# Kernel optimization log

Hardware: AMD Instinct MI355X
Metric: run time of the kernel (lower is better)

Reference implementation:

```python
import jax, jax.numpy as jnp
import numpy as np

N = 100000   # nodes
E = 640000   # directed edges
D = 128      # feature dim
C = 2        # classes


def setup_inputs() -> dict:
    key = jax.random.key(0)
    ks = jax.random.split(key, 7)
    s = 1.0 / np.sqrt(D)
    return {
        "x": jax.random.normal(ks[0], (N, D), jnp.float32),
        "edge_index": jax.random.randint(ks[1], (2, E), 0, N, jnp.int32),
        "W1": jax.random.normal(ks[2], (D, D), jnp.float32) * s,
        "b1": jnp.zeros((D,), jnp.float32),
        "W2": jax.random.normal(ks[3], (D, D), jnp.float32) * s,
        "b2": jnp.zeros((D,), jnp.float32),
        "Wfc": jax.random.normal(ks[4], (D, C), jnp.float32) * s,
        "bfc": jnp.zeros((C,), jnp.float32),
    }


def _gcn_conv(h, src, dst, W, b, n):
    """PyG GCNConv: y = D^{-1/2}(A+I)D^{-1/2} (h @ W) + b."""
    h = h @ W  # [N, D_out]
    loop = jnp.arange(n, dtype=src.dtype)
    s = jnp.concatenate([src, loop])
    d = jnp.concatenate([dst, loop])
    # degree of (A + I) counted at destination
    deg = jax.ops.segment_sum(jnp.ones_like(d, jnp.float32), d, num_segments=n)
    dinv = jax.lax.rsqrt(jnp.maximum(deg, 1.0))  # deg >= 1 via self loops
    norm = dinv[s] * dinv[d]                      # [E+N]
    msg = h[s] * norm[:, None]                    # gather + scale
    out = jax.ops.segment_sum(msg, d, num_segments=n)  # scatter-add
    return out + b


def reference(x, edge_index, W1, b1, W2, b2, Wfc, bfc):
    src, dst = edge_index[0], edge_index[1]
    n = x.shape[0]
    h = jax.nn.relu(_gcn_conv(x, src, dst, W1, b1, n))  # dropout = identity (eval)
    h = jax.nn.relu(_gcn_conv(h, src, dst, W2, b2, n))
    return h @ Wfc + bfc  # [N, 2] logits
```

## Files before the change

### kernel.cpp

```cpp
#include <hip/hip_runtime.h>
#include <hip/hip_bf16.h>

#define D 128

typedef __bf16 bf16x8 __attribute__((ext_vector_type(8)));
typedef float f32x4 __attribute__((ext_vector_type(4)));



__global__ void prep_kernel(const float* __restrict__ W1, const float* __restrict__ W2,
                            __bf16* __restrict__ pw, int* __restrict__ counts, int n) {
    int b = blockIdx.x;
    if (b < 128) {
        int t = b * 256 + threadIdx.x;
        int which = t >> 14, idx = t & 16383;
        const float* W = which ? W2 : W1;
        float w = W[idx];
        int k = idx >> 7, nn = idx & 127;
        int ks = which ? (((k & 15) << 3) | (k >> 4)) : k;
        int ntile = nn >> 4, nl = nn & 15;
        int kchunk = ks >> 5, quad = (ks >> 3) & 3, j = ks & 7;
        int o = (((ntile * 4 + kchunk) * 64 + quad * 16 + nl) << 3) + j;
        pw[(size_t)which * 16384 + o] = (__bf16)w;
    } else {
        int i0 = (b - 128) * 1024 + threadIdx.x * 4;
        if (i0 + 4 <= n) {
            *(int4*)(counts + i0) = make_int4(0, 0, 0, 0);
        } else {
            for (int i = i0; i < n; i++) counts[i] = 0;
        }
    }
}


__global__ void mega1_kernel(const float* __restrict__ X, const __bf16* __restrict__ PW,
                             __bf16* __restrict__ Zs, int nrows, int gb,
                             const int* __restrict__ dst, int* __restrict__ counts,
                             int* __restrict__ eoff, int e) {
    __shared__ bf16x8 sB[2048];
    int b = blockIdx.x;
    if (b >= gb) {
        int i0 = ((b - gb) * 256 + threadIdx.x) * 4;
        if (i0 + 4 <= e) {
            int4 d4 = *(const int4*)(dst + i0);
            int4 o;
            o.x = atomicAdd(&counts[d4.x], 1);
            o.y = atomicAdd(&counts[d4.y], 1);
            o.z = atomicAdd(&counts[d4.z], 1);
            o.w = atomicAdd(&counts[d4.w], 1);
            *(int4*)(eoff + i0) = o;
        } else {
            for (int i = i0; i < e; i++) eoff[i] = atomicAdd(&counts[dst[i]], 1);
        }
        return;
    }
    int t = threadIdx.x;
    const bf16x8* PW8 = (const bf16x8*)PW;
#pragma unroll
    for (int i = 0; i < 8; i++) sB[t + 256 * i] = PW8[t + 256 * i];

    int wave = t >> 6, lane = t & 63;
    int qm = lane & 15, quad = lane >> 4;
    int r0 = b * 64 + wave * 16;
    int row = r0 + qm;
    bool valid = row < nrows;
    const float* xr = X + (size_t)row * D + quad * 8;

    bf16x8 ahi[4], alo[4];
#pragma unroll
    for (int c = 0; c < 4; c++) {
        float4 zf = {0.f, 0.f, 0.f, 0.f};
        float4 xa = valid ? ((const float4*)(xr + c * 32))[0] : zf;
        float4 xb = valid ? ((const float4*)(xr + c * 32))[1] : zf;
        float xs[8] = {xa.x, xa.y, xa.z, xa.w, xb.x, xb.y, xb.z, xb.w};
        bf16x8 h, l;
#pragma unroll
        for (int j = 0; j < 8; j++) {
            float v = xs[j];
            __bf16 hh = (__bf16)v;
            h[j] = hh;
            l[j] = (__bf16)(v - (float)hh);
        }
        ahi[c] = h; alo[c] = l;
    }

    f32x4 acc[8];
#pragma unroll
    for (int nt = 0; nt < 8; nt++) acc[nt] = (f32x4){0.f, 0.f, 0.f, 0.f};

    __syncthreads();

#pragma unroll
    for (int c = 0; c < 4; c++) {
#pragma unroll
        for (int nt = 0; nt < 8; nt++) {
            bf16x8 bb = sB[(nt * 4 + c) * 64 + lane];
            acc[nt] = __builtin_amdgcn_mfma_f32_16x16x32_bf16(ahi[c], bb, acc[nt], 0, 0, 0);
            acc[nt] = __builtin_amdgcn_mfma_f32_16x16x32_bf16(alo[c], bb, acc[nt], 0, 0, 0);
        }
    }

#pragma unroll
    for (int reg = 0; reg < 4; reg++) {
        int orow = r0 + quad * 4 + reg;
        if (orow < nrows) {
            bf16x8 o;
#pragma unroll
            for (int nt = 0; nt < 8; nt++) o[nt] = (__bf16)acc[nt][reg];
            *(bf16x8*)(Zs + (size_t)orow * D + qm * 8) = o;
        }
    }
}


__global__ void scan_part(const int* __restrict__ counts, int* __restrict__ partial, int n) {
    __shared__ int sm[256];
    int b = blockIdx.x, t = threadIdx.x;
    int base = b * 2048 + t * 8;
    int s = 0;
#pragma unroll
    for (int j = 0; j < 8; j++) { int idx = base + j; if (idx < n) s += counts[idx]; }
    sm[t] = s; __syncthreads();
    for (int off = 128; off > 0; off >>= 1) { if (t < off) sm[t] += sm[t + off]; __syncthreads(); }
    if (t == 0) partial[b] = sm[0];
}

__global__ void scan_top(int* partial, int nb) {
    __shared__ int sm[256];
    int t = threadIdx.x;
    int v = (t < nb) ? partial[t] : 0;
    sm[t] = v; __syncthreads();
    for (int off = 1; off < 256; off <<= 1) {
        int u = (t >= off) ? sm[t - off] : 0;
        __syncthreads();
        sm[t] += u;
        __syncthreads();
    }
    if (t < nb) partial[t] = sm[t] - v;
}

__global__ void scan_down(const int* __restrict__ counts, const int* __restrict__ blockoff,
                          int* __restrict__ row_ptr, float* __restrict__ dinv, int n) {
    __shared__ int sm[256];
    int b = blockIdx.x, t = threadIdx.x;
    int base = b * 2048 + t * 8;
    int c[8], local[8];
    int s = 0;
#pragma unroll
    for (int j = 0; j < 8; j++) {
        int idx = base + j;
        c[j] = (idx < n) ? counts[idx] : 0;
        local[j] = s; s += c[j];
        if (idx < n) dinv[idx] = rsqrtf((float)(c[j] + 1));
    }
    sm[t] = s; __syncthreads();
    int own = s;
    for (int off = 1; off < 256; off <<= 1) {
        int u = (t >= off) ? sm[t - off] : 0;
        __syncthreads();
        sm[t] += u;
        __syncthreads();
    }
    int basev = blockoff[b] + sm[t] - own;
#pragma unroll
    for (int j = 0; j < 8; j++) { int idx = base + j; if (idx < n) row_ptr[idx] = basev + local[j]; }
}


__global__ void fill_kernel(const int* __restrict__ src, const int* __restrict__ dst,
                            const int* __restrict__ row_ptr, const int* __restrict__ eoff,
                            const float* __restrict__ dinv, int2* __restrict__ csr, int e) {
    int i0 = (blockIdx.x * 256 + threadIdx.x) * 4;
    if (i0 + 4 <= e) {
        int4 s4 = *(const int4*)(src + i0);
        int4 d4 = *(const int4*)(dst + i0);
        int4 o4 = *(const int4*)(eoff + i0);
        int p0 = row_ptr[d4.x] + o4.x;
        int p1 = row_ptr[d4.y] + o4.y;
        int p2 = row_ptr[d4.z] + o4.z;
        int p3 = row_ptr[d4.w] + o4.w;
        float w0 = dinv[s4.x] * dinv[d4.x];
        float w1 = dinv[s4.y] * dinv[d4.y];
        float w2 = dinv[s4.z] * dinv[d4.z];
        float w3 = dinv[s4.w] * dinv[d4.w];
        csr[p0] = make_int2(s4.x, __float_as_int(w0));
        csr[p1] = make_int2(s4.y, __float_as_int(w1));
        csr[p2] = make_int2(s4.z, __float_as_int(w2));
        csr[p3] = make_int2(s4.w, __float_as_int(w3));
    } else {
        for (int i = i0; i < e; i++) {
            int s = src[i], d = dst[i];
            int pos = row_ptr[d] + eoff[i];
            csr[pos] = make_int2(s, __float_as_int(dinv[s] * dinv[d]));
        }
    }
}


__global__ void gemm2_mfma(const __bf16* __restrict__ Hs, const __bf16* __restrict__ PW,
                           __bf16* __restrict__ Zs, int nrows) {
    __shared__ bf16x8 sB[2048];
    int t = threadIdx.x;
    const bf16x8* PW8 = (const bf16x8*)PW;
#pragma unroll
    for (int i = 0; i < 8; i++) sB[t + 256 * i] = PW8[t + 256 * i];

    int wave = t >> 6, lane = t & 63;
    int qm = lane & 15, quad = lane >> 4;
    int r0 = blockIdx.x * 64 + wave * 16;
    int row = r0 + qm;
    bool valid = row < nrows;
    const __bf16* hr = Hs + (size_t)row * D + quad * 8;

    bf16x8 a[4];
#pragma unroll
    for (int c = 0; c < 4; c++) {
        bf16x8 z8 = {};
        a[c] = valid ? *(const bf16x8*)(hr + c * 32) : z8;
    }

    f32x4 acc[8];
#pragma unroll
    for (int nt = 0; nt < 8; nt++) acc[nt] = (f32x4){0.f, 0.f, 0.f, 0.f};

    __syncthreads();

#pragma unroll
    for (int c = 0; c < 4; c++) {
#pragma unroll
        for (int nt = 0; nt < 8; nt++) {
            bf16x8 b = sB[(nt * 4 + c) * 64 + lane];
            acc[nt] = __builtin_amdgcn_mfma_f32_16x16x32_bf16(a[c], b, acc[nt], 0, 0, 0);
        }
    }

#pragma unroll
    for (int reg = 0; reg < 4; reg++) {
        int orow = r0 + quad * 4 + reg;
        if (orow < nrows) {
            bf16x8 o;
#pragma unroll
            for (int nt = 0; nt < 8; nt++) o[nt] = (__bf16)acc[nt][reg];
            *(bf16x8*)(Zs + (size_t)orow * D + qm * 8) = o;
        }
    }
}


__global__ void agg1_kernel(const __bf16* __restrict__ Zs, const int* __restrict__ row_ptr,
                            const int* __restrict__ counts, const int2* __restrict__ csr,
                            const float* __restrict__ dinv, const float* __restrict__ bias,
                            __bf16* __restrict__ Hs, int n) {
    int t = blockIdx.x * 256 + threadIdx.x;
    int v = t >> 4, c = t & 15;
    if (v >= n) return;
    float dv = dinv[v];
    const bf16x8* Z8 = (const bf16x8*)Zs;
    bf16x8 zc = Z8[(size_t)v * 16 + c];
    float sw = dv * dv;
    float acc[8];
#pragma unroll
    for (int j = 0; j < 8; j++) acc[j] = (float)zc[j] * sw;
    int start = row_ptr[v], cnt = counts[v];
    int i = 0;
    for (; i + 4 <= cnt; i += 4) {
        int2 e0 = csr[start + i], e1 = csr[start + i + 1];
        int2 e2 = csr[start + i + 2], e3 = csr[start + i + 3];
        bf16x8 m0 = Z8[(size_t)e0.x * 16 + c];
        bf16x8 m1 = Z8[(size_t)e1.x * 16 + c];
        bf16x8 m2 = Z8[(size_t)e2.x * 16 + c];
        bf16x8 m3 = Z8[(size_t)e3.x * 16 + c];
        float w0 = __int_as_float(e0.y), w1 = __int_as_float(e1.y);
        float w2 = __int_as_float(e2.y), w3 = __int_as_float(e3.y);
#pragma unroll
        for (int j = 0; j < 8; j++) acc[j] = fmaf(w0, (float)m0[j], acc[j]);
#pragma unroll
        for (int j = 0; j < 8; j++) acc[j] = fmaf(w1, (float)m1[j], acc[j]);
#pragma unroll
        for (int j = 0; j < 8; j++) acc[j] = fmaf(w2, (float)m2[j], acc[j]);
#pragma unroll
        for (int j = 0; j < 8; j++) acc[j] = fmaf(w3, (float)m3[j], acc[j]);
    }
    for (; i < cnt; i++) {
        int2 e0 = csr[start + i];
        float w0 = __int_as_float(e0.y);
        bf16x8 m0 = Z8[(size_t)e0.x * 16 + c];
#pragma unroll
        for (int j = 0; j < 8; j++) acc[j] = fmaf(w0, (float)m0[j], acc[j]);
    }
    bf16x8 o;
#pragma unroll
    for (int j = 0; j < 8; j++) o[j] = (__bf16)fmaxf(acc[j] + bias[j * 16 + c], 0.f);
    ((bf16x8*)Hs)[(size_t)v * 16 + c] = o;
}


__global__ void agg2_fc_kernel(const __bf16* __restrict__ Zs, const int* __restrict__ row_ptr,
                               const int* __restrict__ counts, const int2* __restrict__ csr,
                               const float* __restrict__ dinv, const float* __restrict__ bias,
                               const float* __restrict__ Wfc, const float* __restrict__ bfc,
                               float* __restrict__ out, int n) {
    int t = blockIdx.x * 256 + threadIdx.x;
    int v = t >> 4, c = t & 15;
    if (v >= n) return;
    float dv = dinv[v];
    const bf16x8* Z8 = (const bf16x8*)Zs;
    bf16x8 zc = Z8[(size_t)v * 16 + c];
    float sw = dv * dv;
    float acc[8];
#pragma unroll
    for (int j = 0; j < 8; j++) acc[j] = (float)zc[j] * sw;
    int start = row_ptr[v], cnt = counts[v];
    int i = 0;
    for (; i + 4 <= cnt; i += 4) {
        int2 e0 = csr[start + i], e1 = csr[start + i + 1];
        int2 e2 = csr[start + i + 2], e3 = csr[start + i + 3];
        bf16x8 m0 = Z8[(size_t)e0.x * 16 + c];
        bf16x8 m1 = Z8[(size_t)e1.x * 16 + c];
        bf16x8 m2 = Z8[(size_t)e2.x * 16 + c];
        bf16x8 m3 = Z8[(size_t)e3.x * 16 + c];
        float w0 = __int_as_float(e0.y), w1 = __int_as_float(e1.y);
        float w2 = __int_as_float(e2.y), w3 = __int_as_float(e3.y);
#pragma unroll
        for (int j = 0; j < 8; j++) acc[j] = fmaf(w0, (float)m0[j], acc[j]);
#pragma unroll
        for (int j = 0; j < 8; j++) acc[j] = fmaf(w1, (float)m1[j], acc[j]);
#pragma unroll
        for (int j = 0; j < 8; j++) acc[j] = fmaf(w2, (float)m2[j], acc[j]);
#pragma unroll
        for (int j = 0; j < 8; j++) acc[j] = fmaf(w3, (float)m3[j], acc[j]);
    }
    for (; i < cnt; i++) {
        int2 e0 = csr[start + i];
        float w0 = __int_as_float(e0.y);
        bf16x8 m0 = Z8[(size_t)e0.x * 16 + c];
#pragma unroll
        for (int j = 0; j < 8; j++) acc[j] = fmaf(w0, (float)m0[j], acc[j]);
    }
    float a0 = 0.f, a1 = 0.f;
#pragma unroll
    for (int j = 0; j < 8; j++) {
        int p = j * 16 + c;
        float hj = fmaxf(acc[j] + bias[p], 0.f);
        a0 = fmaf(hj, Wfc[p * 2], a0);
        a1 = fmaf(hj, Wfc[p * 2 + 1], a1);
    }
#pragma unroll
    for (int off = 8; off > 0; off >>= 1) {
        a0 += __shfl_down(a0, off, 16);
        a1 += __shfl_down(a1, off, 16);
    }
    if (c == 0) {
        out[(size_t)v * 2 + 0] = a0 + bfc[0];
        out[(size_t)v * 2 + 1] = a1 + bfc[1];
    }
}


extern "C" void kernel_launch(void* const* d_in, const int* in_sizes, int n_in,
                              void* d_out, int out_size, void* d_ws, size_t ws_size,
                              hipStream_t stream) {
    const float* x   = (const float*)d_in[0];
    const int*   ei  = (const int*)d_in[1];
    const float* W1  = (const float*)d_in[2];
    const float* b1  = (const float*)d_in[3];
    const float* W2  = (const float*)d_in[4];
    const float* b2  = (const float*)d_in[5];
    const float* Wfc = (const float*)d_in[6];
    const float* bfc = (const float*)d_in[7];
    float* out = (float*)d_out;

    int n = in_sizes[0] / D;
    int e = in_sizes[1] / 2;
    const int* src = ei;
    const int* dst = ei + e;

    char* ws = (char*)d_ws;
    size_t nb = (size_t)n * 4;
    int*    counts  = (int*)(ws);
    float*  dinv    = (float*)(ws + nb);
    int*    rowptr  = (int*)(ws + 2 * nb);
    int*    partial = (int*)(ws + 3 * nb);
    int*    eoff    = (int*)(ws + 3 * nb + 1024);
    int2*   csr     = (int2*)(ws + 3 * nb + 1024 + (size_t)e * 4);
    __bf16* pw      = (__bf16*)(ws + 3 * nb + 1024 + (size_t)e * 12);
    __bf16* z1      = (__bf16*)(ws + 3 * nb + 1024 + (size_t)e * 12 + 65536);
    __bf16* h1      = z1 + (size_t)n * D;
    __bf16* z2      = h1 + (size_t)n * D;

    int nzb = (n + 1023) / 1024;
    int e4b = ((e + 3) / 4 + 255) / 256;
    int sb  = (n + 2047) / 2048;
    int gb  = (n + 63) / 64;
    int ab  = ((n * 16) + 255) / 256;

    prep_kernel<<<128 + nzb, 256, 0, stream>>>(W1, W2, pw, counts, n);
    mega1_kernel<<<gb + e4b, 256, 0, stream>>>(x, pw, z1, n, gb, dst, counts, eoff, e);
    scan_part<<<sb, 256, 0, stream>>>(counts, partial, n);
    scan_top<<<1, 256, 0, stream>>>(partial, sb);
    scan_down<<<sb, 256, 0, stream>>>(counts, partial, rowptr, dinv, n);
    fill_kernel<<<e4b, 256, 0, stream>>>(src, dst, rowptr, eoff, dinv, csr, e);

    agg1_kernel<<<ab, 256, 0, stream>>>(z1, rowptr, counts, csr, dinv, b1, h1, n);
    gemm2_mfma<<<gb, 256, 0, stream>>>(h1, pw + 16384, z2, n);
    agg2_fc_kernel<<<ab, 256, 0, stream>>>(z2, rowptr, counts, csr, dinv, b2, Wfc, bfc, out, n);
}
```

Before: 240.6 us.

## Build CSR via dst-bucketed edge partition with shared-memory counting

Replaces per-node global atomic counting and random CSR scatter with a two-level scheme. Edges are first bucketed by destination range into 64 fixed-capacity buckets. Per-bucket blocks then count degrees and fill the CSR using shared-memory atomics. CSR entries shrink to source index only, and the aggregation kernels recompute the edge weight from dinv. This adds redundant bucket scans, a fixed bucket capacity that skewed inputs could overflow, and an extra dinv gather per edge.

```diff
diff --git a/kernel.cpp b/kernel.cpp
--- a/kernel.cpp
+++ b/kernel.cpp
@@ -2,6 +2,8 @@
 #include <hip/hip_bf16.h>
 
 #define D 128
+#define NBUCKET 64
+#define BCAP 16384
 
 typedef __bf16 bf16x8 __attribute__((ext_vector_type(8)));
 typedef float f32x4 __attribute__((ext_vector_type(4)));
@@ -9,7 +11,7 @@
 
 
 __global__ void prep_kernel(const float* __restrict__ W1, const float* __restrict__ W2,
-                            __bf16* __restrict__ pw, int* __restrict__ counts, int n) {
+                            __bf16* __restrict__ pw, int* __restrict__ bucket_cursor) {
     int b = blockIdx.x;
     if (b < 128) {
         int t = b * 256 + threadIdx.x;
@@ -23,38 +25,50 @@
         int o = (((ntile * 4 + kchunk) * 64 + quad * 16 + nl) << 3) + j;
         pw[(size_t)which * 16384 + o] = (__bf16)w;
     } else {
-        int i0 = (b - 128) * 1024 + threadIdx.x * 4;
-        if (i0 + 4 <= n) {
-            *(int4*)(counts + i0) = make_int4(0, 0, 0, 0);
-        } else {
-            for (int i = i0; i < n; i++) counts[i] = 0;
-        }
+        if (threadIdx.x < NBUCKET) bucket_cursor[threadIdx.x] = 0;
     }
 }
 
 
 __global__ void mega1_kernel(const float* __restrict__ X, const __bf16* __restrict__ PW,
                              __bf16* __restrict__ Zs, int nrows, int gb,
-                             const int* __restrict__ dst, int* __restrict__ counts,
-                             int* __restrict__ eoff, int e) {
-    __shared__ bf16x8 sB[2048];
+                             const int* __restrict__ src, const int* __restrict__ dst,
+                             int* __restrict__ bucket_cursor, int2* __restrict__ bucket_edges,
+                             int e, int bucketW) {
+    __shared__ __align__(16) char smem[32768];
+    int t = threadIdx.x;
     int b = blockIdx.x;
     if (b >= gb) {
-        int i0 = ((b - gb) * 256 + threadIdx.x) * 4;
+        int* hist = (int*)smem;
+        int* gbase = hist + 64;
+        if (t < NBUCKET) hist[t] = 0;
+        __syncthreads();
+        int i0 = ((b - gb) * 256 + t) * 4;
+        int sv[4], dv[4], bk[4], ls[4];
+        int nv = 0;
         if (i0 + 4 <= e) {
+            int4 s4 = *(const int4*)(src + i0);
             int4 d4 = *(const int4*)(dst + i0);
-            int4 o;
-            o.x = atomicAdd(&counts[d4.x], 1);
-            o.y = atomicAdd(&counts[d4.y], 1);
-            o.z = atomicAdd(&counts[d4.z], 1);
-            o.w = atomicAdd(&counts[d4.w], 1);
-            *(int4*)(eoff + i0) = o;
+            sv[0] = s4.x; sv[1] = s4.y; sv[2] = s4.z; sv[3] = s4.w;
+            dv[0] = d4.x; dv[1] = d4.y; dv[2] = d4.z; dv[3] = d4.w;
+            nv = 4;
         } else {
-            for (int i = i0; i < e; i++) eoff[i] = atomicAdd(&counts[dst[i]], 1);
+            for (int i = i0; i < e; i++) { sv[nv] = src[i]; dv[nv] = dst[i]; nv++; }
+        }
+        for (int u = 0; u < nv; u++) {
+            bk[u] = dv[u] / bucketW;
+            ls[u] = atomicAdd(&hist[bk[u]], 1);
+        }
+        __syncthreads();
+        if (t < NBUCKET) gbase[t] = atomicAdd(&bucket_cursor[t], hist[t]);
+        __syncthreads();
+        for (int u = 0; u < nv; u++) {
+            int pos = bk[u] * BCAP + gbase[bk[u]] + ls[u];
+            bucket_edges[pos] = make_int2(sv[u], dv[u]);
         }
         return;
     }
-    int t = threadIdx.x;
+    bf16x8* sB = (bf16x8*)smem;
     const bf16x8* PW8 = (const bf16x8*)PW;
 #pragma unroll
     for (int i = 0; i < 8; i++) sB[t + 256 * i] = PW8[t + 256 * i];
@@ -110,6 +124,30 @@
             *(bf16x8*)(Zs + (size_t)orow * D + qm * 8) = o;
         }
     }
+}
+
+
+__global__ void count_kernel(const int2* __restrict__ bucket_edges,
+                             const int* __restrict__ bucket_cursor,
+                             int* __restrict__ counts, int n, int bucketW, int subW) {
+    __shared__ int bins[400];
+    int b = blockIdx.x, t = threadIdx.x;
+    int bk = b >> 2, j = b & 3;
+    int ns = bk * bucketW + j * subW;
+    int be = min((bk + 1) * bucketW, n);
+    int ne = min(ns + subW, be);
+    if (ns >= ne) return;
+    int w = ne - ns;
+    for (int i = t; i < w; i += 256) bins[i] = 0;
+    __syncthreads();
+    int m = bucket_cursor[bk];
+    const int2* eb = bucket_edges + (size_t)bk * BCAP;
+    for (int i = t; i < m; i += 256) {
+        int d = eb[i].y;
+        if (d >= ns && d < ne) atomicAdd(&bins[d - ns], 1);
+    }
+    __syncthreads();
+    for (int i = t; i < w; i += 256) counts[ns + i] = bins[i];
 }
 
 
@@ -167,31 +205,27 @@
 }
 
 
-__global__ void fill_kernel(const int* __restrict__ src, const int* __restrict__ dst,
-                            const int* __restrict__ row_ptr, const int* __restrict__ eoff,
-                            const float* __restrict__ dinv, int2* __restrict__ csr, int e) {
-    int i0 = (blockIdx.x * 256 + threadIdx.x) * 4;
-    if (i0 + 4 <= e) {
-        int4 s4 = *(const int4*)(src + i0);
-        int4 d4 = *(const int4*)(dst + i0);
-        int4 o4 = *(const int4*)(eoff + i0);
-        int p0 = row_ptr[d4.x] + o4.x;
-        int p1 = row_ptr[d4.y] + o4.y;
-        int p2 = row_ptr[d4.z] + o4.z;
-        int p3 = row_ptr[d4.w] + o4.w;
-        float w0 = dinv[s4.x] * dinv[d4.x];
-        float w1 = dinv[s4.y] * dinv[d4.y];
-        float w2 = dinv[s4.z] * dinv[d4.z];
-        float w3 = dinv[s4.w] * dinv[d4.w];
-        csr[p0] = make_int2(s4.x, __float_as_int(w0));
-        csr[p1] = make_int2(s4.y, __float_as_int(w1));
-        csr[p2] = make_int2(s4.z, __float_as_int(w2));
-        csr[p3] = make_int2(s4.w, __float_as_int(w3));
-    } else {
-        for (int i = i0; i < e; i++) {
-            int s = src[i], d = dst[i];
-            int pos = row_ptr[d] + eoff[i];
-            csr[pos] = make_int2(s, __float_as_int(dinv[s] * dinv[d]));
+__global__ void fill_kernel(const int2* __restrict__ bucket_edges,
+                            const int* __restrict__ bucket_cursor,
+                            const int* __restrict__ row_ptr, int* __restrict__ csr,
+                            int n, int bucketW, int subW) {
+    __shared__ int cur[400];
+    int b = blockIdx.x, t = threadIdx.x;
+    int bk = b >> 2, j = b & 3;
+    int ns = bk * bucketW + j * subW;
+    int be = min((bk + 1) * bucketW, n);
+    int ne = min(ns + subW, be);
+    if (ns >= ne) return;
+    int w = ne - ns;
+    for (int i = t; i < w; i += 256) cur[i] = row_ptr[ns + i];
+    __syncthreads();
+    int m = bucket_cursor[bk];
+    const int2* eb = bucket_edges + (size_t)bk * BCAP;
+    for (int i = t; i < m; i += 256) {
+        int2 ed = eb[i];
+        if (ed.y >= ns && ed.y < ne) {
+            int pos = atomicAdd(&cur[ed.y - ns], 1);
+            csr[pos] = ed.x;
         }
     }
 }
@@ -248,7 +282,7 @@
 
 
 __global__ void agg1_kernel(const __bf16* __restrict__ Zs, const int* __restrict__ row_ptr,
-                            const int* __restrict__ counts, const int2* __restrict__ csr,
+                            const int* __restrict__ counts, const int* __restrict__ csr,
                             const float* __restrict__ dinv, const float* __restrict__ bias,
                             __bf16* __restrict__ Hs, int n) {
     int t = blockIdx.x * 256 + threadIdx.x;
@@ -264,14 +298,14 @@
     int start = row_ptr[v], cnt = counts[v];
     int i = 0;
     for (; i + 4 <= cnt; i += 4) {
-        int2 e0 = csr[start + i], e1 = csr[start + i + 1];
-        int2 e2 = csr[start + i + 2], e3 = csr[start + i + 3];
-        bf16x8 m0 = Z8[(size_t)e0.x * 16 + c];
-        bf16x8 m1 = Z8[(size_t)e1.x * 16 + c];
-        bf16x8 m2 = Z8[(size_t)e2.x * 16 + c];
-        bf16x8 m3 = Z8[(size_t)e3.x * 16 + c];
-        float w0 = __int_as_float(e0.y), w1 = __int_as_float(e1.y);
-        float w2 = __int_as_float(e2.y), w3 = __int_as_float(e3.y);
+        int s0 = csr[start + i], s1 = csr[start + i + 1];
+        int s2 = csr[start + i + 2], s3 = csr[start + i + 3];
+        bf16x8 m0 = Z8[(size_t)s0 * 16 + c];
+        bf16x8 m1 = Z8[(size_t)s1 * 16 + c];
+        bf16x8 m2 = Z8[(size_t)s2 * 16 + c];
+        bf16x8 m3 = Z8[(size_t)s3 * 16 + c];
+        float w0 = dinv[s0] * dv, w1 = dinv[s1] * dv;
+        float w2 = dinv[s2] * dv, w3 = dinv[s3] * dv;
 #pragma unroll
         for (int j = 0; j < 8; j++) acc[j] = fmaf(w0, (float)m0[j], acc[j]);
 #pragma unroll
@@ -282,9 +316,9 @@
         for (int j = 0; j < 8; j++) acc[j] = fmaf(w3, (float)m3[j], acc[j]);
     }
     for (; i < cnt; i++) {
-        int2 e0 = csr[start + i];
-        float w0 = __int_as_float(e0.y);
-        bf16x8 m0 = Z8[(size_t)e0.x * 16 + c];
+        int s0 = csr[start + i];
+        float w0 = dinv[s0] * dv;
+        bf16x8 m0 = Z8[(size_t)s0 * 16 + c];
 #pragma unroll
         for (int j = 0; j < 8; j++) acc[j] = fmaf(w0, (float)m0[j], acc[j]);
     }
@@ -296,7 +330,7 @@
 
 
 __global__ void agg2_fc_kernel(const __bf16* __restrict__ Zs, const int* __restrict__ row_ptr,
-                               const int* __restrict__ counts, const int2* __restrict__ csr,
+                               const int* __restrict__ counts, const int* __restrict__ csr,
                                const float* __restrict__ dinv, const float* __restrict__ bias,
                                const float* __restrict__ Wfc, const float* __restrict__ bfc,
                                float* __restrict__ out, int n) {
@@ -313,14 +347,14 @@
     int start = row_ptr[v], cnt = counts[v];
     int i = 0;
     for (; i + 4 <= cnt; i += 4) {
-        int2 e0 = csr[start + i], e1 = csr[start + i + 1];
-        int2 e2 = csr[start + i + 2], e3 = csr[start + i + 3];
-        bf16x8 m0 = Z8[(size_t)e0.x * 16 + c];
-        bf16x8 m1 = Z8[(size_t)e1.x * 16 + c];
-        bf16x8 m2 = Z8[(size_t)e2.x * 16 + c];
-        bf16x8 m3 = Z8[(size_t)e3.x * 16 + c];
-        float w0 = __int_as_float(e0.y), w1 = __int_as_float(e1.y);
-        float w2 = __int_as_float(e2.y), w3 = __int_as_float(e3.y);
+        int s0 = csr[start + i], s1 = csr[start + i + 1];
+        int s2 = csr[start + i + 2], s3 = csr[start + i + 3];
+        bf16x8 m0 = Z8[(size_t)s0 * 16 + c];
+        bf16x8 m1 = Z8[(size_t)s1 * 16 + c];
+        bf16x8 m2 = Z8[(size_t)s2 * 16 + c];
+        bf16x8 m3 = Z8[(size_t)s3 * 16 + c];
+        float w0 = dinv[s0] * dv, w1 = dinv[s1] * dv;
+        float w2 = dinv[s2] * dv, w3 = dinv[s3] * dv;
 #pragma unroll
         for (int j = 0; j < 8; j++) acc[j] = fmaf(w0, (float)m0[j], acc[j]);
 #pragma unroll
@@ -331,9 +365,9 @@
         for (int j = 0; j < 8; j++) acc[j] = fmaf(w3, (float)m3[j], acc[j]);
     }
     for (; i < cnt; i++) {
-        int2 e0 = csr[start + i];
-        float w0 = __int_as_float(e0.y);
-        bf16x8 m0 = Z8[(size_t)e0.x * 16 + c];
+        int s0 = csr[start + i];
+        float w0 = dinv[s0] * dv;
+        bf16x8 m0 = Z8[(size_t)s0 * 16 + c];
 #pragma unroll
         for (int j = 0; j < 8; j++) acc[j] = fmaf(w0, (float)m0[j], acc[j]);
     }
@@ -375,31 +409,37 @@
     const int* src = ei;
     const int* dst = ei + e;
 
+    int bucketW = (n + NBUCKET - 1) / NBUCKET;
+    int subW = (bucketW + 3) / 4;
+
     char* ws = (char*)d_ws;
     size_t nb = (size_t)n * 4;
     int*    counts  = (int*)(ws);
     float*  dinv    = (float*)(ws + nb);
     int*    rowptr  = (int*)(ws + 2 * nb);
     int*    partial = (int*)(ws + 3 * nb);
-    int*    eoff    = (int*)(ws + 3 * nb + 1024);
-    int2*   csr     = (int2*)(ws + 3 * nb + 1024 + (size_t)e * 4);
-    __bf16* pw      = (__bf16*)(ws + 3 * nb + 1024 + (size_t)e * 12);
-    __bf16* z1      = (__bf16*)(ws + 3 * nb + 1024 + (size_t)e * 12 + 65536);
+    int*    bcur    = (int*)(ws + 3 * nb + 1024);
+    int2*   bedges  = (int2*)(ws + 3 * nb + 2048);
+    size_t  off1    = 3 * nb + 2048 + (size_t)NBUCKET * BCAP * 8;
+    int*    csr     = (int*)(ws + off1);
+    __bf16* pw      = (__bf16*)(ws + off1 + (size_t)e * 4);
+    __bf16* z1      = (__bf16*)(ws + off1 + (size_t)e * 4 + 65536);
     __bf16* h1      = z1 + (size_t)n * D;
     __bf16* z2      = h1 + (size_t)n * D;
 
-    int nzb = (n + 1023) / 1024;
-    int e4b = ((e + 3) / 4 + 255) / 256;
+    int eab = ((e + 3) / 4 + 255) / 256;
     int sb  = (n + 2047) / 2048;
     int gb  = (n + 63) / 64;
     int ab  = ((n * 16) + 255) / 256;
 
-    prep_kernel<<<128 + nzb, 256, 0, stream>>>(W1, W2, pw, counts, n);
-    mega1_kernel<<<gb + e4b, 256, 0, stream>>>(x, pw, z1, n, gb, dst, counts, eoff, e);
+    prep_kernel<<<129, 256, 0, stream>>>(W1, W2, pw, bcur);
+    mega1_kernel<<<gb + eab, 256, 0, stream>>>(x, pw, z1, n, gb, src, dst,
+                                               bcur, bedges, e, bucketW);
+    count_kernel<<<256, 256, 0, stream>>>(bedges, bcur, counts, n, bucketW, subW);
     scan_part<<<sb, 256, 0, stream>>>(counts, partial, n);
     scan_top<<<1, 256, 0, stream>>>(partial, sb);
     scan_down<<<sb, 256, 0, stream>>>(counts, partial, rowptr, dinv, n);
-    fill_kernel<<<e4b, 256, 0, stream>>>(src, dst, rowptr, eoff, dinv, csr, e);
+    fill_kernel<<<256, 256, 0, stream>>>(bedges, bcur, rowptr, csr, n, bucketW, subW);
 
     agg1_kernel<<<ab, 256, 0, stream>>>(z1, rowptr, counts, csr, dinv, b1, h1, n);
     gemm2_mfma<<<gb, 256, 0, stream>>>(h1, pw + 16384, z2, n);
```

After: 241.5 us. No clear change (+0.4%).
